# Optimization experiments

Hardware: AMD Instinct MI355X
Metric: run time of the kernel (lower is better)

The kernel has to match this reference:

```python
import jax, jax.numpy as jnp
import numpy as np

B, L, T, IN, H, OUT = 1024, 64, 128, 13, 64, 13
NEG = -1e30


def gru_step(x, h, Wih, Whh, bih, bhh):
    # PyTorch GRU cell: gates ordered (r, z, n)
    gi = x @ Wih.T + bih          # [B, 3H]
    gh = h @ Whh.T + bhh          # [B, 3H]
    ir, iz, inn = jnp.split(gi, 3, axis=-1)
    hr, hz, hn = jnp.split(gh, 3, axis=-1)
    r = jax.nn.sigmoid(ir + hr)
    z = jax.nn.sigmoid(iz + hz)
    n = jnp.tanh(inn + r * hn)
    return (1.0 - z) * n + z * h


def setup_inputs() -> dict:
    key = jax.random.key(0)
    ks = jax.random.split(key, 10)
    s = float(1.0 / np.sqrt(H))
    x = jax.random.normal(ks[0], (B, L, IN), jnp.float32)
    lengths = jax.random.randint(ks[1], (B,), 1, L + 1).at[0].set(L)
    Wih = jax.random.uniform(ks[2], (3 * H, IN), jnp.float32, -s, s)
    Whh = jax.random.uniform(ks[3], (3 * H, H), jnp.float32, -s, s)
    bih = jax.random.uniform(ks[4], (3 * H,), jnp.float32, -s, s)
    bhh = jax.random.uniform(ks[5], (3 * H,), jnp.float32, -s, s)
    Wf = jax.random.uniform(ks[6], (OUT, H), jnp.float32, -s, s)
    bf = jax.random.uniform(ks[7], (OUT,), jnp.float32, -s, s)
    Wa = jax.random.uniform(ks[8], (H, H), jnp.float32, -s, s)
    ba = jax.random.uniform(ks[9], (H,), jnp.float32, -s, s)
    return dict(x=x, lengths=lengths, output_length=T, Wih=Wih, Whh=Whh,
                bih=bih, bhh=bhh, Wf=Wf, bf=bf, Wa=Wa, ba=ba)


def reference(x, lengths, output_length, Wih, Whh, bih, bhh, Wf, bf, Wa, ba):
    b, l = x.shape[0], x.shape[1]
    xT = jnp.swapaxes(x, 0, 1)                        # [L, B, IN]
    h0 = jnp.zeros((b, H), x.dtype)

    # Encoder: masked GRU emulating pack_padded/pad_packed semantics:
    # hidden frozen past each sequence's length; outputs zero past length.
    def enc(h, inp):
        t, xt = inp
        hn = gru_step(xt, h, Wih, Whh, bih, bhh)
        valid = (t < lengths)[:, None]
        h = jnp.where(valid, hn, h)
        return h, jnp.where(valid, hn, 0.0)

    h, outs = jax.lax.scan(enc, h0, (jnp.arange(l), xT))
    # output[:, -1, :] of the padded output (zeros for seqs shorter than max)
    nin = outs[-1] @ Wf.T + bf                        # [B, OUT]

    Tn = output_length
    buf0 = jnp.zeros((Tn, b, H), x.dtype)             # growing past-prediction buffer

    def dec(carry, t):
        h, buf, nin = carry
        hn = gru_step(nin, h, Wih, Whh, bih, bhh)     # output_lstm == hidden (1 layer, 1 step)
        # attention recomputed over all past predictions (softmax over time axis)
        logits = jnp.einsum('tbh,gh->tbg', buf, Wa) + ba      # [T, B, H]
        logits = jnp.where((jnp.arange(Tn) < t)[:, None, None], logits, NEG)
        w = jax.nn.softmax(logits, axis=0)
        o = hn + jnp.sum(w * buf, axis=0)             # at t=0 buffer is all zeros -> +0
        y = o @ Wf.T + bf
        return (hn, buf.at[t].set(o), y), y

    _, ys = jax.lax.scan(dec, (h, buf0, nin), jnp.arange(Tn))
    return jnp.swapaxes(ys, 0, 1)                     # [B, T, OUT]
```

## Files before the change

### kernel.cpp

```cpp
#include <hip/hip_runtime.h>
#include <stdint.h>
#include <math.h>

#define BATCH 1024
#define SEQL  64
#define TDEC  128
#define NIN   13
#define NH    64
#define NOUT  13

typedef _Float16 h2 __attribute__((ext_vector_type(2)));
typedef __fp16   g2 __attribute__((ext_vector_type(2)));

union FU  { uint32_t u; float f; };
union HU  { uint16_t u; _Float16 h; };
union H2U { uint32_t u; h2 h; g2 g; };

__device__ __forceinline__ float bf2f(uint16_t v) { FU t; t.u = ((uint32_t)v) << 16; return t.f; }
__device__ __forceinline__ float hf2f(uint16_t v) { HU t; t.u = v; return (float)t.h; }

__device__ __forceinline__ float ldf(const void* p, long i, int mode) {
    if (mode == 1) return bf2f(((const uint16_t*)p)[i]);
    if (mode == 2) return hf2f(((const uint16_t*)p)[i]);
    return ((const float*)p)[i];
}

__device__ __forceinline__ bool pass_stats(const void* p, int n, int lane, int mode,
                                           float band_lo, float band_hi, float max_ok) {
    int m = (n + 1) / 2;
    int cnt = (m < 64) ? m : 64;
    bool ok_max = true, in_band = false;
    if (lane < cnt) {
        long pos = 2L * (((long)lane * m) / cnt);
        float v = (mode == 1) ? bf2f(((const uint16_t*)p)[pos])
                              : hf2f(((const uint16_t*)p)[pos]);
        float a = fabsf(v);
        ok_max  = (a <= max_ok);
        in_band = (a >= band_lo && a <= band_hi);
    }
    bool allmax = __all(ok_max);
    int nb = (int)__popcll(__ballot(in_band));
    int need = cnt / 4; if (need < 1) need = 1;
    return allmax && (nb >= need);
}
__device__ __forceinline__ int detect(const void* p, int n, int lane,
                                      float band_lo, float band_hi, float max_ok) {
    if (pass_stats(p, n, lane, 1, band_lo, band_hi, max_ok)) return 1;
    if (pass_stats(p, n, lane, 2, band_lo, band_hi, max_ok)) return 2;
    return 0;
}
__device__ __forceinline__ bool detect_len64(const int* p, int lane) {
    int v = p[2 * lane + 1];
    return __all(v == 0);
}

__device__ __forceinline__ float dot2(h2 a, h2 b, float c) {
#if __has_builtin(__builtin_amdgcn_fdot2)
    return __builtin_amdgcn_fdot2(a, b, c, false);
#else
    return c + (float)a[0] * (float)b[0] + (float)a[1] * (float)b[1];
#endif
}
__device__ __forceinline__ uint32_t pku(float a, float b) {
    H2U t; t.g = __builtin_amdgcn_cvt_pkrtz(a, b); return t.u;
}
__device__ __forceinline__ h2 uh(uint32_t u) { H2U t; t.u = u; return t.h; }
__device__ __forceinline__ float rcp_(float x) { return __builtin_amdgcn_rcpf(x); }
__device__ __forceinline__ float exp2_(float x) {
#if __has_builtin(__builtin_amdgcn_exp2f)
    return __builtin_amdgcn_exp2f(x);
#else
    return __expf(x * 0.69314718056f);
#endif
}
__device__ __forceinline__ float sigm2(float xs)  { return rcp_(1.0f + exp2_(-xs)); }
__device__ __forceinline__ float tanh2(float xs)  { return 1.0f - 2.0f * rcp_(exp2_(xs) + 1.0f); }

__device__ __forceinline__ float swap1(float v) {
    FU a; a.f = v;
    FU b; b.u = (uint32_t)__builtin_amdgcn_mov_dpp((int)a.u, 0xB1, 0xF, 0xF, true);
    return b.f;
}

#define BCAST32(vreg, dst)                                                 \
    {                                                                      \
        uint32_t _pr = pku((vreg), swap1(vreg));                           \
        _Pragma("unroll")                                                  \
        for (int _k = 0; _k < 32; ++_k)                                    \
            (dst)[_k] = __builtin_amdgcn_readlane(_pr, 2 * _k);            \
    }

__global__ __launch_bounds__(64, 1)
void gru_attn_kernel(const void* __restrict__ x, const int* __restrict__ lengths,
                     const void* __restrict__ Wih, const void* __restrict__ Whh,
                     const void* __restrict__ bih, const void* __restrict__ bhh,
                     const void* __restrict__ Wf, const void* __restrict__ bfv,
                     const void* __restrict__ Wa, const void* __restrict__ ba,
                     float* __restrict__ out)
{
    const int b = blockIdx.x;
    const int j = threadIdx.x;

    const int dX   = detect(x,   BATCH * SEQL * NIN, j, 0.25f, 4.0f, 16.0f);
    const int dWih = detect(Wih, 3 * NH * NIN, j, 0.04f, 0.13f, 0.14f);
    const int dWhh = detect(Whh, 3 * NH * NH,  j, 0.04f, 0.13f, 0.14f);
    const int dBih = detect(bih, 3 * NH,       j, 0.04f, 0.13f, 0.14f);
    const int dBhh = detect(bhh, 3 * NH,       j, 0.04f, 0.13f, 0.14f);
    const int dWf  = detect(Wf,  NOUT * NH,    j, 0.04f, 0.13f, 0.14f);
    const int dBf  = detect(bfv, NOUT,         j, 0.04f, 0.13f, 0.14f);
    const int dWa  = detect(Wa,  NH * NH,      j, 0.04f, 0.13f, 0.14f);
    const int dBa  = detect(ba,  NH,           j, 0.04f, 0.13f, 0.14f);
    const bool len64 = detect_len64(lengths, j);

    const float L2E  = 1.44269504089f;
    const float L2E2 = 2.88539008177f;

    h2 wihr[7], wihz[7], wihn[7];
    h2 whhr[32], whhz[32], whhn[32];
    h2 wap[32], wfp[32];

#pragma unroll
    for (int k = 0; k < 7; ++k) {
        float a0 = ldf(Wih, (0 * NH + j) * NIN + 2 * k, dWih);
        float a1 = (2 * k + 1 < NIN) ? ldf(Wih, (0 * NH + j) * NIN + 2 * k + 1, dWih) : 0.0f;
        wihr[k] = uh(pku(a0 * L2E, a1 * L2E));
        float b0 = ldf(Wih, (1 * NH + j) * NIN + 2 * k, dWih);
        float b1 = (2 * k + 1 < NIN) ? ldf(Wih, (1 * NH + j) * NIN + 2 * k + 1, dWih) : 0.0f;
        wihz[k] = uh(pku(b0 * L2E, b1 * L2E));
        float c0 = ldf(Wih, (2 * NH + j) * NIN + 2 * k, dWih);
        float c1 = (2 * k + 1 < NIN) ? ldf(Wih, (2 * NH + j) * NIN + 2 * k + 1, dWih) : 0.0f;
        wihn[k] = uh(pku(c0 * L2E2, c1 * L2E2));
    }
    const int jf = (j < NOUT) ? j : 0;
#pragma unroll
    for (int k = 0; k < 32; ++k) {
        whhr[k] = uh(pku(ldf(Whh, (0 * NH + j) * NH + 2 * k, dWhh) * L2E,
                         ldf(Whh, (0 * NH + j) * NH + 2 * k + 1, dWhh) * L2E));
        whhz[k] = uh(pku(ldf(Whh, (1 * NH + j) * NH + 2 * k, dWhh) * L2E,
                         ldf(Whh, (1 * NH + j) * NH + 2 * k + 1, dWhh) * L2E));
        whhn[k] = uh(pku(ldf(Whh, (2 * NH + j) * NH + 2 * k, dWhh) * L2E2,
                         ldf(Whh, (2 * NH + j) * NH + 2 * k + 1, dWhh) * L2E2));
        wap[k]  = uh(pku(ldf(Wa, j * NH + 2 * k, dWa) * L2E,
                         ldf(Wa, j * NH + 2 * k + 1, dWa) * L2E));
        wfp[k]  = uh(pku(ldf(Wf, jf * NH + 2 * k, dWf),
                         ldf(Wf, jf * NH + 2 * k + 1, dWf)));
    }

    const float bcr = (ldf(bih, j, dBih)      + ldf(bhh, j, dBhh))      * L2E;
    const float bcz = (ldf(bih, NH + j, dBih) + ldf(bhh, NH + j, dBhh)) * L2E;
    const float bni = ldf(bih, 2 * NH + j, dBih) * L2E2;
    const float bnh = ldf(bhh, 2 * NH + j, dBhh) * L2E2;
    const float baj = ldf(ba, j, dBa) * L2E;
    const float bfj = ldf(bfv, jf, dBf);
    const int len = len64 ? lengths[2 * b] : lengths[b];

    uint32_t xp[7];
    {
        const long base = ((long)b * SEQL + j) * NIN;
        float v[14];
#pragma unroll
        for (int k = 0; k < NIN; ++k) v[k] = ldf(x, base + k, dX);
        v[13] = 0.0f;
#pragma unroll
        for (int p = 0; p < 7; ++p) xp[p] = pku(v[2 * p], v[2 * p + 1]);
    }

    float h = 0.0f;
    float out_last = 0.0f;

    uint32_t hpk[32];
#pragma unroll
    for (int k = 0; k < 32; ++k) hpk[k] = 0u;

    float gir, giz, gin;
    {
        uint32_t xw[7];
#pragma unroll
        for (int p = 0; p < 7; ++p) xw[p] = __builtin_amdgcn_readlane(xp[p], 0);
        float r0 = 0.0f, z0 = 0.0f, n0 = 0.0f;
#pragma unroll
        for (int p = 0; p < 7; ++p) {
            h2 xv = uh(xw[p]);
            r0 = dot2(wihr[p], xv, r0);
            z0 = dot2(wihz[p], xv, z0);
            n0 = dot2(wihn[p], xv, n0);
        }
        gir = r0; giz = z0; gin = n0;
    }

#pragma unroll 1
    for (int t = 0; t < SEQL; ++t) {
        float arA = bcr, azA = bcz, hnA = bnh;
        float arB = 0.0f, azB = 0.0f, hnB = 0.0f;
        float arC = 0.0f, azC = 0.0f, hnC = 0.0f;
        float arD = 0.0f, azD = 0.0f, hnD = 0.0f;
#pragma unroll
        for (int k = 0; k < 32; k += 4) {
            h2 h0 = uh(hpk[k]), h1 = uh(hpk[k + 1]), h2v = uh(hpk[k + 2]), h3 = uh(hpk[k + 3]);
            arA = dot2(whhr[k],     h0, arA); azA = dot2(whhz[k],     h0, azA); hnA = dot2(whhn[k],     h0, hnA);
            arB = dot2(whhr[k + 1], h1, arB); azB = dot2(whhz[k + 1], h1, azB); hnB = dot2(whhn[k + 1], h1, hnB);
            arC = dot2(whhr[k + 2], h2v, arC); azC = dot2(whhz[k + 2], h2v, azC); hnC = dot2(whhn[k + 2], h2v, hnC);
            arD = dot2(whhr[k + 3], h3, arD); azD = dot2(whhz[k + 3], h3, azD); hnD = dot2(whhn[k + 3], h3, hnD);
        }

        float girN = 0.0f, gizN = 0.0f, ginN = 0.0f;
        {
            uint32_t xwN[7];
#pragma unroll
            for (int p = 0; p < 7; ++p)
                xwN[p] = __builtin_amdgcn_readlane(xp[p], (t + 1) & 63);
#pragma unroll
            for (int p = 0; p < 7; ++p) {
                h2 xv = uh(xwN[p]);
                girN = dot2(wihr[p], xv, girN);
                gizN = dot2(wihz[p], xv, gizN);
                ginN = dot2(wihn[p], xv, ginN);
            }
        }

        float ar = ((arA + arB) + (arC + arD)) + gir;
        float az = ((azA + azB) + (azC + azD)) + giz;
        float hna = (hnA + hnB) + (hnC + hnD);
        float an = bni + gin;
        float r = sigm2(ar);
        float z = sigm2(az);
        float n = tanh2(an + r * hna);
        float hnew = n + z * (h - n);
        bool upd = (t < len);
        h = upd ? hnew : h;
        if (t == SEQL - 1) out_last = upd ? hnew : 0.0f;
        BCAST32(h, hpk);
        gir = girN; giz = gizN; gin = ginN;
    }

    uint32_t ypk0[7];
    {
        uint32_t opk[32];
        BCAST32(out_last, opk);
        float nA = bfj, nB = 0.0f, nC = 0.0f, nD = 0.0f;
#pragma unroll
        for (int k = 0; k < 32; k += 4) {
            nA = dot2(wfp[k],     uh(opk[k]),     nA);
            nB = dot2(wfp[k + 1], uh(opk[k + 1]), nB);
            nC = dot2(wfp[k + 2], uh(opk[k + 2]), nC);
            nD = dot2(wfp[k + 3], uh(opk[k + 3]), nD);
        }
        float nv = (nA + nB) + (nC + nD);
        float nz = (j < NOUT) ? nv : 0.0f;
        uint32_t pr = pku(nz, swap1(nz));
#pragma unroll
        for (int k = 0; k < 7; ++k) ypk0[k] = __builtin_amdgcn_readlane(pr, 2 * k);
    }

    float m = -1e30f, Zs = 0.0f, num = 0.0f;
    float o_prev;

    {
        float arA = bcr, azA = bcz, hnA = bnh, anA = bni;
        float arB = 0.0f, azB = 0.0f, hnB = 0.0f;
        float arC = 0.0f, azC = 0.0f, hnC = 0.0f;
        float arD = 0.0f, azD = 0.0f, hnD = 0.0f;
#pragma unroll
        for (int k = 0; k < 32; k += 4) {
            h2 h0 = uh(hpk[k]), h1 = uh(hpk[k + 1]), h2v = uh(hpk[k + 2]), h3 = uh(hpk[k + 3]);
            arA = dot2(whhr[k],     h0, arA); azA = dot2(whhz[k],     h0, azA); hnA = dot2(whhn[k],     h0, hnA);
            arB = dot2(whhr[k + 1], h1, arB); azB = dot2(whhz[k + 1], h1, azB); hnB = dot2(whhn[k + 1], h1, hnB);
            arC = dot2(whhr[k + 2], h2v, arC); azC = dot2(whhz[k + 2], h2v, azC); hnC = dot2(whhn[k + 2], h2v, hnC);
            arD = dot2(whhr[k + 3], h3, arD); azD = dot2(whhz[k + 3], h3, azD); hnD = dot2(whhn[k + 3], h3, hnD);
        }
#pragma unroll
        for (int p = 0; p < 7; ++p) {
            h2 xv = uh(ypk0[p]);
            arB = dot2(wihr[p], xv, arB);
            azB = dot2(wihz[p], xv, azB);
            anA = dot2(wihn[p], xv, anA);
        }
        float ar = (arA + arB) + (arC + arD);
        float az = (azA + azB) + (azC + azD);
        float hna = (hnA + hnB) + (hnC + hnD);
        float r = sigm2(ar);
        float z = sigm2(az);
        float n = tanh2(anA + r * hna);
        float hnew = n + z * (h - n);
        h = hnew;
        BCAST32(hnew, hpk);
        o_prev = hnew;
    }

#pragma unroll 1
    for (int t = 1; t < TDEC; ++t) {
        uint32_t opk[32];
        BCAST32(o_prev, opk);

        float arA = bcr, azA = bcz, hnA = bnh, anA = bni;
        float arB = 0.0f, azB = 0.0f, hnB = 0.0f;
        float arC = 0.0f, azC = 0.0f, hnC = 0.0f;
        float arD = 0.0f, azD = 0.0f, hnD = 0.0f;
#pragma unroll
        for (int k = 0; k < 32; k += 4) {
            h2 h0 = uh(hpk[k]), h1 = uh(hpk[k + 1]), h2v = uh(hpk[k + 2]), h3 = uh(hpk[k + 3]);
            arA = dot2(whhr[k],     h0, arA); azA = dot2(whhz[k],     h0, azA); hnA = dot2(whhn[k],     h0, hnA);
            arB = dot2(whhr[k + 1], h1, arB); azB = dot2(whhz[k + 1], h1, azB); hnB = dot2(whhn[k + 1], h1, hnB);
            arC = dot2(whhr[k + 2], h2v, arC); azC = dot2(whhz[k + 2], h2v, azC); hnC = dot2(whhn[k + 2], h2v, hnC);
            arD = dot2(whhr[k + 3], h3, arD); azD = dot2(whhz[k + 3], h3, azD); hnD = dot2(whhn[k + 3], h3, hnD);
        }

        float yA = bfj, yB = 0.0f, yC = 0.0f, yD = 0.0f;
#pragma unroll
        for (int k = 0; k < 32; k += 4) {
            yA = dot2(wfp[k],     uh(opk[k]),     yA);
            yB = dot2(wfp[k + 1], uh(opk[k + 1]), yB);
            yC = dot2(wfp[k + 2], uh(opk[k + 2]), yC);
            yD = dot2(wfp[k + 3], uh(opk[k + 3]), yD);
        }
        float yv = (yA + yB) + (yC + yD);
        if (j < NOUT) out[((size_t)b * TDEC + (t - 1)) * NOUT + j] = yv;

        uint32_t ypk[7];
        {
            float yz = (j < NOUT) ? yv : 0.0f;
            uint32_t pr = pku(yz, swap1(yz));
#pragma unroll
            for (int k = 0; k < 7; ++k) ypk[k] = __builtin_amdgcn_readlane(pr, 2 * k);
        }
#pragma unroll
        for (int p = 0; p < 7; ++p) {
            h2 xv = uh(ypk[p]);
            arB = dot2(wihr[p], xv, arB);
            azB = dot2(wihz[p], xv, azB);
            anA = dot2(wihn[p], xv, anA);
        }

        float sA = baj, sB = 0.0f, sC = 0.0f, sD = 0.0f;
#pragma unroll
        for (int k = 0; k < 32; k += 4) {
            sA = dot2(wap[k],     uh(opk[k]),     sA);
            sB = dot2(wap[k + 1], uh(opk[k + 1]), sB);
            sC = dot2(wap[k + 2], uh(opk[k + 2]), sC);
            sD = dot2(wap[k + 3], uh(opk[k + 3]), sD);
        }
        float s_ = (sA + sB) + (sC + sD);
        float mn = fmaxf(m, s_);
        float al = exp2_(m - mn);
        float pp = exp2_(s_ - mn);
        Zs  = Zs * al + pp;
        num = num * al + pp * o_prev;
        m = mn;

        float ar = (arA + arB) + (arC + arD);
        float az = (azA + azB) + (azC + azD);
        float hna = (hnA + hnB) + (hnC + hnD);
        float r_ = sigm2(ar);
        float z_ = sigm2(az);
        float n_ = tanh2(anA + r_ * hna);
        float hnew = n_ + z_ * (h - n_);
        h = hnew;

        float attn = num * rcp_(Zs);
        float o_ = hnew + attn;
        BCAST32(hnew, hpk);
        o_prev = o_;
    }

    {
        uint32_t opk[32];
        BCAST32(o_prev, opk);
        float yA = bfj, yB = 0.0f, yC = 0.0f, yD = 0.0f;
#pragma unroll
        for (int k = 0; k < 32; k += 4) {
            yA = dot2(wfp[k],     uh(opk[k]),     yA);
            yB = dot2(wfp[k + 1], uh(opk[k + 1]), yB);
            yC = dot2(wfp[k + 2], uh(opk[k + 2]), yC);
            yD = dot2(wfp[k + 3], uh(opk[k + 3]), yD);
        }
        float yv = (yA + yB) + (yC + yD);
        if (j < NOUT) out[((size_t)b * TDEC + (TDEC - 1)) * NOUT + j] = yv;
    }
}

extern "C" void kernel_launch(void* const* d_in, const int* in_sizes, int n_in,
                              void* d_out, int out_size, void* d_ws, size_t ws_size,
                              hipStream_t stream) {
    (void)in_sizes; (void)n_in; (void)out_size; (void)d_ws; (void)ws_size;
    const void* x      = d_in[0];
    const int* lengths = (const int*)d_in[1];
    const void* Wih = d_in[3];
    const void* Whh = d_in[4];
    const void* bih = d_in[5];
    const void* bhh = d_in[6];
    const void* Wf  = d_in[7];
    const void* bf  = d_in[8];
    const void* Wa  = d_in[9];
    const void* ba  = d_in[10];
    float* out = (float*)d_out;

    gru_attn_kernel<<<dim3(BATCH), dim3(64), 0, stream>>>(
        x, lengths, Wih, Whh, bih, bhh, Wf, bf, Wa, ba, out);
}
```

Baseline: 231.4 us.

## Broadcast decoder output via LDS and interleave attention/output dots with recurrence

Replaces the readlane broadcast of each decoder step's output with packed fp16 writes to a small shared-memory buffer read back as vector loads. The half-precision dot products for the attention score and output projection are interleaved with the recurrent dot products. The encoder loop is simplified to compute the input projection inline with unroll 2 instead of software-pipelining it. The intent is to cut the 32 serial readlanes per decoder step and improve instruction-level parallelism, but no barrier is placed between the LDS write and the next read. That relies on single-wave execution and risks a race.

```diff
diff --git a/kernel.cpp b/kernel.cpp
--- a/kernel.cpp
+++ b/kernel.cpp
@@ -90,6 +90,23 @@
             (dst)[_k] = __builtin_amdgcn_readlane(_pr, 2 * _k);            \
     }
 
+#define BWRITE(DSTB, V)                                                    \
+    {                                                                      \
+        float _w  = swap1(V);                                              \
+        float _lo = odd ? _w  : (V);                                       \
+        float _hi = odd ? (V) : _w;                                        \
+        (DSTB)[jhalf] = pku(_lo, _hi);                                     \
+    }
+#define BREAD(SRC, DST)                                                    \
+    {                                                                      \
+        _Pragma("unroll")                                                  \
+        for (int _k = 0; _k < 32; _k += 4) {                               \
+            uint4 _q = *(const uint4*)((SRC) + _k);                        \
+            (DST)[_k]     = _q.x; (DST)[_k + 1] = _q.y;                    \
+            (DST)[_k + 2] = _q.z; (DST)[_k + 3] = _q.w;                    \
+        }                                                                  \
+    }
+
 __global__ __launch_bounds__(64, 1)
 void gru_attn_kernel(const void* __restrict__ x, const int* __restrict__ lengths,
                      const void* __restrict__ Wih, const void* __restrict__ Whh,
@@ -100,6 +117,10 @@
 {
     const int b = blockIdx.x;
     const int j = threadIdx.x;
+    const bool odd = j & 1;
+    const int jhalf = j >> 1;
+
+    __shared__ __align__(16) uint32_t ob[32];
 
     const int dX   = detect(x,   BATCH * SEQL * NIN, j, 0.25f, 4.0f, 16.0f);
     const int dWih = detect(Wih, 3 * NH * NIN, j, 0.04f, 0.13f, 0.14f);
@@ -169,28 +190,15 @@
     float out_last = 0.0f;
 
     uint32_t hpk[32];
-#pragma unroll
-    for (int k = 0; k < 32; ++k) hpk[k] = 0u;
-
-    float gir, giz, gin;
-    {
+    BCAST32(h, hpk);
+
+#pragma unroll 2
+    for (int t = 0; t < SEQL; ++t) {
         uint32_t xw[7];
 #pragma unroll
-        for (int p = 0; p < 7; ++p) xw[p] = __builtin_amdgcn_readlane(xp[p], 0);
-        float r0 = 0.0f, z0 = 0.0f, n0 = 0.0f;
-#pragma unroll
-        for (int p = 0; p < 7; ++p) {
-            h2 xv = uh(xw[p]);
-            r0 = dot2(wihr[p], xv, r0);
-            z0 = dot2(wihz[p], xv, z0);
-            n0 = dot2(wihn[p], xv, n0);
-        }
-        gir = r0; giz = z0; gin = n0;
-    }
-
-#pragma unroll 1
-    for (int t = 0; t < SEQL; ++t) {
-        float arA = bcr, azA = bcz, hnA = bnh;
+        for (int p = 0; p < 7; ++p) xw[p] = __builtin_amdgcn_readlane(xp[p], t);
+
+        float arA = bcr, azA = bcz, hnA = bnh, anA = bni;
         float arB = 0.0f, azB = 0.0f, hnB = 0.0f;
         float arC = 0.0f, azC = 0.0f, hnC = 0.0f;
         float arD = 0.0f, azD = 0.0f, hnD = 0.0f;
@@ -202,38 +210,27 @@
             arC = dot2(whhr[k + 2], h2v, arC); azC = dot2(whhz[k + 2], h2v, azC); hnC = dot2(whhn[k + 2], h2v, hnC);
             arD = dot2(whhr[k + 3], h3, arD); azD = dot2(whhz[k + 3], h3, azD); hnD = dot2(whhn[k + 3], h3, hnD);
         }
-
-        float girN = 0.0f, gizN = 0.0f, ginN = 0.0f;
-        {
-            uint32_t xwN[7];
-#pragma unroll
-            for (int p = 0; p < 7; ++p)
-                xwN[p] = __builtin_amdgcn_readlane(xp[p], (t + 1) & 63);
-#pragma unroll
-            for (int p = 0; p < 7; ++p) {
-                h2 xv = uh(xwN[p]);
-                girN = dot2(wihr[p], xv, girN);
-                gizN = dot2(wihz[p], xv, gizN);
-                ginN = dot2(wihn[p], xv, ginN);
-            }
-        }
-
-        float ar = ((arA + arB) + (arC + arD)) + gir;
-        float az = ((azA + azB) + (azC + azD)) + giz;
+#pragma unroll
+        for (int p = 0; p < 7; ++p) {
+            h2 xv = uh(xw[p]);
+            arB = dot2(wihr[p], xv, arB);
+            azB = dot2(wihz[p], xv, azB);
+            anA = dot2(wihn[p], xv, anA);
+        }
+        float ar = (arA + arB) + (arC + arD);
+        float az = (azA + azB) + (azC + azD);
         float hna = (hnA + hnB) + (hnC + hnD);
-        float an = bni + gin;
         float r = sigm2(ar);
         float z = sigm2(az);
-        float n = tanh2(an + r * hna);
+        float n = tanh2(anA + r * hna);
         float hnew = n + z * (h - n);
         bool upd = (t < len);
         h = upd ? hnew : h;
         if (t == SEQL - 1) out_last = upd ? hnew : 0.0f;
         BCAST32(h, hpk);
-        gir = girN; giz = gizN; gin = ginN;
-    }
-
-    uint32_t ypk0[7];
+    }
+
+    uint32_t ypk[7];
     {
         uint32_t opk[32];
         BCAST32(out_last, opk);
@@ -249,7 +246,7 @@
         float nz = (j < NOUT) ? nv : 0.0f;
         uint32_t pr = pku(nz, swap1(nz));
 #pragma unroll
-        for (int k = 0; k < 7; ++k) ypk0[k] = __builtin_amdgcn_readlane(pr, 2 * k);
+        for (int k = 0; k < 7; ++k) ypk[k] = __builtin_amdgcn_readlane(pr, 2 * k);
     }
 
     float m = -1e30f, Zs = 0.0f, num = 0.0f;
@@ -270,7 +267,7 @@
         }
 #pragma unroll
         for (int p = 0; p < 7; ++p) {
-            h2 xv = uh(ypk0[p]);
+            h2 xv = uh(ypk[p]);
             arB = dot2(wihr[p], xv, arB);
             azB = dot2(wihz[p], xv, azB);
             anA = dot2(wihn[p], xv, anA);
@@ -285,19 +282,21 @@
         h = hnew;
         BCAST32(hnew, hpk);
         o_prev = hnew;
+        BWRITE(ob, o_prev);
     }
 
 #pragma unroll 1
-    for (int t = 1; t < TDEC; ++t) {
+    for (int t = 0; t < TDEC - 1; ++t) {
         uint32_t opk[32];
-        BCAST32(o_prev, opk);
+        BREAD(ob, opk);
 
         float arA = bcr, azA = bcz, hnA = bnh, anA = bni;
         float arB = 0.0f, azB = 0.0f, hnB = 0.0f;
         float arC = 0.0f, azC = 0.0f, hnC = 0.0f;
         float arD = 0.0f, azD = 0.0f, hnD = 0.0f;
-#pragma unroll
-        for (int k = 0; k < 32; k += 4) {
+
+#pragma unroll
+        for (int k = 0; k < 16; k += 4) {
             h2 h0 = uh(hpk[k]), h1 = uh(hpk[k + 1]), h2v = uh(hpk[k + 2]), h3 = uh(hpk[k + 3]);
             arA = dot2(whhr[k],     h0, arA); azA = dot2(whhz[k],     h0, azA); hnA = dot2(whhn[k],     h0, hnA);
             arB = dot2(whhr[k + 1], h1, arB); azB = dot2(whhz[k + 1], h1, azB); hnB = dot2(whhn[k + 1], h1, hnB);
@@ -305,24 +304,47 @@
             arD = dot2(whhr[k + 3], h3, arD); azD = dot2(whhz[k + 3], h3, azD); hnD = dot2(whhn[k + 3], h3, hnD);
         }
 
+        float sA = baj, sB = 0.0f, sC = 0.0f, sD = 0.0f;
         float yA = bfj, yB = 0.0f, yC = 0.0f, yD = 0.0f;
-#pragma unroll
-        for (int k = 0; k < 32; k += 4) {
+
+#pragma unroll
+        for (int k = 16; k < 32; k += 4) {
+            const int k2 = k - 16;
+            h2 h0 = uh(hpk[k]), h1 = uh(hpk[k + 1]), h2v = uh(hpk[k + 2]), h3 = uh(hpk[k + 3]);
+            h2 o0 = uh(opk[k2]), o1 = uh(opk[k2 + 1]), o2 = uh(opk[k2 + 2]), o3 = uh(opk[k2 + 3]);
+            arA = dot2(whhr[k],     h0, arA); azA = dot2(whhz[k],     h0, azA); hnA = dot2(whhn[k],     h0, hnA);
+            sA = dot2(wap[k2],     o0, sA);  yA = dot2(wfp[k2],     o0, yA);
+            arB = dot2(whhr[k + 1], h1, arB); azB = dot2(whhz[k + 1], h1, azB); hnB = dot2(whhn[k + 1], h1, hnB);
+            sB = dot2(wap[k2 + 1], o1, sB);  yB = dot2(wfp[k2 + 1], o1, yB);
+            arC = dot2(whhr[k + 2], h2v, arC); azC = dot2(whhz[k + 2], h2v, azC); hnC = dot2(whhn[k + 2], h2v, hnC);
+            sC = dot2(wap[k2 + 2], o2, sC);  yC = dot2(wfp[k2 + 2], o2, yC);
+            arD = dot2(whhr[k + 3], h3, arD); azD = dot2(whhz[k + 3], h3, azD); hnD = dot2(whhn[k + 3], h3, hnD);
+            sD = dot2(wap[k2 + 3], o3, sD);  yD = dot2(wfp[k2 + 3], o3, yD);
+        }
+
+#pragma unroll
+        for (int k = 16; k < 32; k += 4) {
             yA = dot2(wfp[k],     uh(opk[k]),     yA);
             yB = dot2(wfp[k + 1], uh(opk[k + 1]), yB);
             yC = dot2(wfp[k + 2], uh(opk[k + 2]), yC);
             yD = dot2(wfp[k + 3], uh(opk[k + 3]), yD);
         }
         float yv = (yA + yB) + (yC + yD);
-        if (j < NOUT) out[((size_t)b * TDEC + (t - 1)) * NOUT + j] = yv;
-
-        uint32_t ypk[7];
         {
             float yz = (j < NOUT) ? yv : 0.0f;
             uint32_t pr = pku(yz, swap1(yz));
 #pragma unroll
             for (int k = 0; k < 7; ++k) ypk[k] = __builtin_amdgcn_readlane(pr, 2 * k);
         }
+
+#pragma unroll
+        for (int k = 16; k < 32; k += 4) {
+            sA = dot2(wap[k],     uh(opk[k]),     sA);
+            sB = dot2(wap[k + 1], uh(opk[k + 1]), sB);
+            sC = dot2(wap[k + 2], uh(opk[k + 2]), sC);
+            sD = dot2(wap[k + 3], uh(opk[k + 3]), sD);
+        }
+
 #pragma unroll
         for (int p = 0; p < 7; ++p) {
             h2 xv = uh(ypk[p]);
@@ -331,14 +353,6 @@
             anA = dot2(wihn[p], xv, anA);
         }
 
-        float sA = baj, sB = 0.0f, sC = 0.0f, sD = 0.0f;
-#pragma unroll
-        for (int k = 0; k < 32; k += 4) {
-            sA = dot2(wap[k],     uh(opk[k]),     sA);
-            sB = dot2(wap[k + 1], uh(opk[k + 1]), sB);
-            sC = dot2(wap[k + 2], uh(opk[k + 2]), sC);
-            sD = dot2(wap[k + 3], uh(opk[k + 3]), sD);
-        }
         float s_ = (sA + sB) + (sC + sD);
         float mn = fmaxf(m, s_);
         float al = exp2_(m - mn);
@@ -346,6 +360,7 @@
         Zs  = Zs * al + pp;
         num = num * al + pp * o_prev;
         m = mn;
+        float attn = num * rcp_(Zs);
 
         float ar = (arA + arB) + (arC + arD);
         float az = (azA + azB) + (azC + azD);
@@ -356,15 +371,17 @@
         float hnew = n_ + z_ * (h - n_);
         h = hnew;
 
-        float attn = num * rcp_(Zs);
         float o_ = hnew + attn;
         BCAST32(hnew, hpk);
+        BWRITE(ob, o_);
         o_prev = o_;
+
+        if (j < NOUT) out[((size_t)b * TDEC + t) * NOUT + j] = yv;
     }
 
     {
         uint32_t opk[32];
-        BCAST32(o_prev, opk);
+        BREAD(ob, opk);
         float yA = bfj, yB = 0.0f, yC = 0.0f, yD = 0.0f;
 #pragma unroll
         for (int k = 0; k < 32; k += 4) {
```

New measurement: 218.5 us. -5.6%, faster.

## Split hidden-dim reduction across two wavefronts with LDS partial-sum exchange

Applied to the files above, without the earlier changes.

Each block now runs two wavefronts, and each one handles half of the 64-wide hidden input dimension for the recurrent, attention and output matvecs. Partial sums are swapped through a double-buffered shared-memory array with a __syncthreads each step. This halves the per-thread dot-product and readlane broadcast work on the serial recurrence critical path. In exchange it adds a block barrier and an LDS round trip per timestep, and it drops the encoder's one-step-ahead input-projection prefetch.

```diff
diff --git a/kernel.cpp b/kernel.cpp
--- a/kernel.cpp
+++ b/kernel.cpp
@@ -82,15 +82,15 @@
     return b.f;
 }
 
-#define BCAST32(vreg, dst)                                                 \
+#define PACKHALF(vreg, dst)                                                \
     {                                                                      \
         uint32_t _pr = pku((vreg), swap1(vreg));                           \
         _Pragma("unroll")                                                  \
-        for (int _k = 0; _k < 32; ++_k)                                    \
-            (dst)[_k] = __builtin_amdgcn_readlane(_pr, 2 * _k);            \
-    }
-
-__global__ __launch_bounds__(64, 1)
+        for (int _k = 0; _k < 16; ++_k)                                    \
+            (dst)[_k] = __builtin_amdgcn_readlane(_pr, kb + 2 * _k);       \
+    }
+
+__global__ __launch_bounds__(128, 1)
 void gru_attn_kernel(const void* __restrict__ x, const int* __restrict__ lengths,
                      const void* __restrict__ Wih, const void* __restrict__ Whh,
                      const void* __restrict__ bih, const void* __restrict__ bhh,
@@ -98,8 +98,12 @@
                      const void* __restrict__ Wa, const void* __restrict__ ba,
                      float* __restrict__ out)
 {
-    const int b = blockIdx.x;
-    const int j = threadIdx.x;
+    const int b  = blockIdx.x;
+    const int j  = threadIdx.x & 63;
+    const int w  = threadIdx.x >> 6;
+    const int kb = w << 5;
+
+    __shared__ __align__(16) float xch[2][2][64][8];
 
     const int dX   = detect(x,   BATCH * SEQL * NIN, j, 0.25f, 4.0f, 16.0f);
     const int dWih = detect(Wih, 3 * NH * NIN, j, 0.04f, 0.13f, 0.14f);
@@ -116,8 +120,8 @@
     const float L2E2 = 2.88539008177f;
 
     h2 wihr[7], wihz[7], wihn[7];
-    h2 whhr[32], whhz[32], whhn[32];
-    h2 wap[32], wfp[32];
+    h2 whhr[16], whhz[16], whhn[16];
+    h2 wap[16], wfp[16];
 
 #pragma unroll
     for (int k = 0; k < 7; ++k) {
@@ -133,17 +137,18 @@
     }
     const int jf = (j < NOUT) ? j : 0;
 #pragma unroll
-    for (int k = 0; k < 32; ++k) {
-        whhr[k] = uh(pku(ldf(Whh, (0 * NH + j) * NH + 2 * k, dWhh) * L2E,
-                         ldf(Whh, (0 * NH + j) * NH + 2 * k + 1, dWhh) * L2E));
-        whhz[k] = uh(pku(ldf(Whh, (1 * NH + j) * NH + 2 * k, dWhh) * L2E,
-                         ldf(Whh, (1 * NH + j) * NH + 2 * k + 1, dWhh) * L2E));
-        whhn[k] = uh(pku(ldf(Whh, (2 * NH + j) * NH + 2 * k, dWhh) * L2E2,
-                         ldf(Whh, (2 * NH + j) * NH + 2 * k + 1, dWhh) * L2E2));
-        wap[k]  = uh(pku(ldf(Wa, j * NH + 2 * k, dWa) * L2E,
-                         ldf(Wa, j * NH + 2 * k + 1, dWa) * L2E));
-        wfp[k]  = uh(pku(ldf(Wf, jf * NH + 2 * k, dWf),
-                         ldf(Wf, jf * NH + 2 * k + 1, dWf)));
+    for (int k = 0; k < 16; ++k) {
+        const int c = kb + 2 * k;
+        whhr[k] = uh(pku(ldf(Whh, (0 * NH + j) * NH + c, dWhh) * L2E,
+                         ldf(Whh, (0 * NH + j) * NH + c + 1, dWhh) * L2E));
+        whhz[k] = uh(pku(ldf(Whh, (1 * NH + j) * NH + c, dWhh) * L2E,
+                         ldf(Whh, (1 * NH + j) * NH + c + 1, dWhh) * L2E));
+        whhn[k] = uh(pku(ldf(Whh, (2 * NH + j) * NH + c, dWhh) * L2E2,
+                         ldf(Whh, (2 * NH + j) * NH + c + 1, dWhh) * L2E2));
+        wap[k]  = uh(pku(ldf(Wa, j * NH + c, dWa) * L2E,
+                         ldf(Wa, j * NH + c + 1, dWa) * L2E));
+        wfp[k]  = uh(pku(ldf(Wf, jf * NH + c, dWf),
+                         ldf(Wf, jf * NH + c + 1, dWf)));
     }
 
     const float bcr = (ldf(bih, j, dBih)      + ldf(bhh, j, dBhh))      * L2E;
@@ -167,214 +172,224 @@
 
     float h = 0.0f;
     float out_last = 0.0f;
-
-    uint32_t hpk[32];
-#pragma unroll
-    for (int k = 0; k < 32; ++k) hpk[k] = 0u;
-
-    float gir, giz, gin;
-    {
-        uint32_t xw[7];
-#pragma unroll
-        for (int p = 0; p < 7; ++p) xw[p] = __builtin_amdgcn_readlane(xp[p], 0);
-        float r0 = 0.0f, z0 = 0.0f, n0 = 0.0f;
-#pragma unroll
-        for (int p = 0; p < 7; ++p) {
-            h2 xv = uh(xw[p]);
-            r0 = dot2(wihr[p], xv, r0);
-            z0 = dot2(wihz[p], xv, z0);
-            n0 = dot2(wihn[p], xv, n0);
-        }
-        gir = r0; giz = z0; gin = n0;
-    }
+    int par = 0;
+
+    uint32_t hpk[16];
+#pragma unroll
+    for (int k = 0; k < 16; ++k) hpk[k] = 0u;
 
 #pragma unroll 1
     for (int t = 0; t < SEQL; ++t) {
-        float arA = bcr, azA = bcz, hnA = bnh;
-        float arB = 0.0f, azB = 0.0f, hnB = 0.0f;
-        float arC = 0.0f, azC = 0.0f, hnC = 0.0f;
-        float arD = 0.0f, azD = 0.0f, hnD = 0.0f;
-#pragma unroll
-        for (int k = 0; k < 32; k += 4) {
+        uint32_t xw[7];
+#pragma unroll
+        for (int p = 0; p < 7; ++p) xw[p] = __builtin_amdgcn_readlane(xp[p], t);
+
+        float arA = 0.f, azA = 0.f, hnA = 0.f;
+        float arB = 0.f, azB = 0.f, hnB = 0.f;
+        float arC = 0.f, azC = 0.f, hnC = 0.f;
+        float arD = 0.f, azD = 0.f, hnD = 0.f;
+#pragma unroll
+        for (int k = 0; k < 16; k += 4) {
             h2 h0 = uh(hpk[k]), h1 = uh(hpk[k + 1]), h2v = uh(hpk[k + 2]), h3 = uh(hpk[k + 3]);
             arA = dot2(whhr[k],     h0, arA); azA = dot2(whhz[k],     h0, azA); hnA = dot2(whhn[k],     h0, hnA);
             arB = dot2(whhr[k + 1], h1, arB); azB = dot2(whhz[k + 1], h1, azB); hnB = dot2(whhn[k + 1], h1, hnB);
             arC = dot2(whhr[k + 2], h2v, arC); azC = dot2(whhz[k + 2], h2v, azC); hnC = dot2(whhn[k + 2], h2v, hnC);
             arD = dot2(whhr[k + 3], h3, arD); azD = dot2(whhz[k + 3], h3, azD); hnD = dot2(whhn[k + 3], h3, hnD);
         }
-
-        float girN = 0.0f, gizN = 0.0f, ginN = 0.0f;
-        {
-            uint32_t xwN[7];
-#pragma unroll
-            for (int p = 0; p < 7; ++p)
-                xwN[p] = __builtin_amdgcn_readlane(xp[p], (t + 1) & 63);
-#pragma unroll
-            for (int p = 0; p < 7; ++p) {
-                h2 xv = uh(xwN[p]);
-                girN = dot2(wihr[p], xv, girN);
-                gizN = dot2(wihz[p], xv, gizN);
-                ginN = dot2(wihn[p], xv, ginN);
-            }
-        }
-
-        float ar = ((arA + arB) + (arC + arD)) + gir;
-        float az = ((azA + azB) + (azC + azD)) + giz;
-        float hna = (hnA + hnB) + (hnC + hnD);
-        float an = bni + gin;
+        float gr = bcr, gz = bcz, gn = bni;
+#pragma unroll
+        for (int p = 0; p < 7; ++p) {
+            h2 xv = uh(xw[p]);
+            gr = dot2(wihr[p], xv, gr);
+            gz = dot2(wihz[p], xv, gz);
+            gn = dot2(wihn[p], xv, gn);
+        }
+
+        float arP = (arA + arB) + (arC + arD);
+        float azP = (azA + azB) + (azC + azD);
+        float hnP = (hnA + hnB) + (hnC + hnD);
+        *(float4*)&xch[par][w][j][0] = make_float4(arP, azP, hnP, 0.f);
+        __syncthreads();
+        float4 q = *(const float4*)&xch[par][w ^ 1][j][0];
+        par ^= 1;
+
+        float ar  = (arP + q.x) + gr;
+        float az  = (azP + q.y) + gz;
+        float hna = (hnP + q.z) + bnh;
         float r = sigm2(ar);
         float z = sigm2(az);
-        float n = tanh2(an + r * hna);
+        float n = tanh2(gn + r * hna);
         float hnew = n + z * (h - n);
         bool upd = (t < len);
         h = upd ? hnew : h;
         if (t == SEQL - 1) out_last = upd ? hnew : 0.0f;
-        BCAST32(h, hpk);
-        gir = girN; giz = gizN; gin = ginN;
-    }
-
-    uint32_t ypk0[7];
+        PACKHALF(h, hpk);
+    }
+
+    uint32_t ypk[7];
     {
-        uint32_t opk[32];
-        BCAST32(out_last, opk);
-        float nA = bfj, nB = 0.0f, nC = 0.0f, nD = 0.0f;
-#pragma unroll
-        for (int k = 0; k < 32; k += 4) {
-            nA = dot2(wfp[k],     uh(opk[k]),     nA);
-            nB = dot2(wfp[k + 1], uh(opk[k + 1]), nB);
-            nC = dot2(wfp[k + 2], uh(opk[k + 2]), nC);
-            nD = dot2(wfp[k + 3], uh(opk[k + 3]), nD);
-        }
-        float nv = (nA + nB) + (nC + nD);
+        uint32_t olk[16];
+        PACKHALF(out_last, olk);
+        float nA = 0.f, nB = 0.f, nC = 0.f, nD = 0.f;
+#pragma unroll
+        for (int k = 0; k < 16; k += 4) {
+            nA = dot2(wfp[k],     uh(olk[k]),     nA);
+            nB = dot2(wfp[k + 1], uh(olk[k + 1]), nB);
+            nC = dot2(wfp[k + 2], uh(olk[k + 2]), nC);
+            nD = dot2(wfp[k + 3], uh(olk[k + 3]), nD);
+        }
+        float nP = (nA + nB) + (nC + nD);
+        xch[par][w][j][0] = nP;
+        __syncthreads();
+        float qn = xch[par][w ^ 1][j][0];
+        par ^= 1;
+        float nv = (nP + qn) + bfj;
         float nz = (j < NOUT) ? nv : 0.0f;
         uint32_t pr = pku(nz, swap1(nz));
 #pragma unroll
-        for (int k = 0; k < 7; ++k) ypk0[k] = __builtin_amdgcn_readlane(pr, 2 * k);
+        for (int k = 0; k < 7; ++k) ypk[k] = __builtin_amdgcn_readlane(pr, 2 * k);
     }
 
     float m = -1e30f, Zs = 0.0f, num = 0.0f;
     float o_prev;
+    uint32_t opk[16];
 
     {
-        float arA = bcr, azA = bcz, hnA = bnh, anA = bni;
-        float arB = 0.0f, azB = 0.0f, hnB = 0.0f;
-        float arC = 0.0f, azC = 0.0f, hnC = 0.0f;
-        float arD = 0.0f, azD = 0.0f, hnD = 0.0f;
-#pragma unroll
-        for (int k = 0; k < 32; k += 4) {
+        float arA = 0.f, azA = 0.f, hnA = 0.f;
+        float arB = 0.f, azB = 0.f, hnB = 0.f;
+        float arC = 0.f, azC = 0.f, hnC = 0.f;
+        float arD = 0.f, azD = 0.f, hnD = 0.f;
+#pragma unroll
+        for (int k = 0; k < 16; k += 4) {
             h2 h0 = uh(hpk[k]), h1 = uh(hpk[k + 1]), h2v = uh(hpk[k + 2]), h3 = uh(hpk[k + 3]);
             arA = dot2(whhr[k],     h0, arA); azA = dot2(whhz[k],     h0, azA); hnA = dot2(whhn[k],     h0, hnA);
             arB = dot2(whhr[k + 1], h1, arB); azB = dot2(whhz[k + 1], h1, azB); hnB = dot2(whhn[k + 1], h1, hnB);
             arC = dot2(whhr[k + 2], h2v, arC); azC = dot2(whhz[k + 2], h2v, azC); hnC = dot2(whhn[k + 2], h2v, hnC);
             arD = dot2(whhr[k + 3], h3, arD); azD = dot2(whhz[k + 3], h3, azD); hnD = dot2(whhn[k + 3], h3, hnD);
         }
+        float gr = bcr, gz = bcz, gn = bni;
 #pragma unroll
         for (int p = 0; p < 7; ++p) {
-            h2 xv = uh(ypk0[p]);
-            arB = dot2(wihr[p], xv, arB);
-            azB = dot2(wihz[p], xv, azB);
-            anA = dot2(wihn[p], xv, anA);
-        }
-        float ar = (arA + arB) + (arC + arD);
-        float az = (azA + azB) + (azC + azD);
-        float hna = (hnA + hnB) + (hnC + hnD);
+            h2 xv = uh(ypk[p]);
+            gr = dot2(wihr[p], xv, gr);
+            gz = dot2(wihz[p], xv, gz);
+            gn = dot2(wihn[p], xv, gn);
+        }
+        float arP = (arA + arB) + (arC + arD);
+        float azP = (azA + azB) + (azC + azD);
+        float hnP = (hnA + hnB) + (hnC + hnD);
+        *(float4*)&xch[par][w][j][0] = make_float4(arP, azP, hnP, 0.f);
+        __syncthreads();
+        float4 q = *(const float4*)&xch[par][w ^ 1][j][0];
+        par ^= 1;
+        float ar  = (arP + q.x) + gr;
+        float az  = (azP + q.y) + gz;
+        float hna = (hnP + q.z) + bnh;
         float r = sigm2(ar);
         float z = sigm2(az);
-        float n = tanh2(anA + r * hna);
+        float n = tanh2(gn + r * hna);
         float hnew = n + z * (h - n);
         h = hnew;
-        BCAST32(hnew, hpk);
         o_prev = hnew;
+        PACKHALF(hnew, hpk);
+        PACKHALF(o_prev, opk);
     }
 
 #pragma unroll 1
     for (int t = 1; t < TDEC; ++t) {
-        uint32_t opk[32];
-        BCAST32(o_prev, opk);
-
-        float arA = bcr, azA = bcz, hnA = bnh, anA = bni;
-        float arB = 0.0f, azB = 0.0f, hnB = 0.0f;
-        float arC = 0.0f, azC = 0.0f, hnC = 0.0f;
-        float arD = 0.0f, azD = 0.0f, hnD = 0.0f;
-#pragma unroll
-        for (int k = 0; k < 32; k += 4) {
+        float arA = 0.f, azA = 0.f, hnA = 0.f;
+        float arB = 0.f, azB = 0.f, hnB = 0.f;
+        float arC = 0.f, azC = 0.f, hnC = 0.f;
+        float arD = 0.f, azD = 0.f, hnD = 0.f;
+#pragma unroll
+        for (int k = 0; k < 16; k += 4) {
             h2 h0 = uh(hpk[k]), h1 = uh(hpk[k + 1]), h2v = uh(hpk[k + 2]), h3 = uh(hpk[k + 3]);
             arA = dot2(whhr[k],     h0, arA); azA = dot2(whhz[k],     h0, azA); hnA = dot2(whhn[k],     h0, hnA);
             arB = dot2(whhr[k + 1], h1, arB); azB = dot2(whhz[k + 1], h1, azB); hnB = dot2(whhn[k + 1], h1, hnB);
             arC = dot2(whhr[k + 2], h2v, arC); azC = dot2(whhz[k + 2], h2v, azC); hnC = dot2(whhn[k + 2], h2v, hnC);
             arD = dot2(whhr[k + 3], h3, arD); azD = dot2(whhz[k + 3], h3, azD); hnD = dot2(whhn[k + 3], h3, hnD);
         }
-
-        float yA = bfj, yB = 0.0f, yC = 0.0f, yD = 0.0f;
-#pragma unroll
-        for (int k = 0; k < 32; k += 4) {
-            yA = dot2(wfp[k],     uh(opk[k]),     yA);
-            yB = dot2(wfp[k + 1], uh(opk[k + 1]), yB);
-            yC = dot2(wfp[k + 2], uh(opk[k + 2]), yC);
-            yD = dot2(wfp[k + 3], uh(opk[k + 3]), yD);
-        }
-        float yv = (yA + yB) + (yC + yD);
-        if (j < NOUT) out[((size_t)b * TDEC + (t - 1)) * NOUT + j] = yv;
-
-        uint32_t ypk[7];
+        float sA = 0.f, sB = 0.f, sC = 0.f, sD = 0.f;
+        float yA = 0.f, yB = 0.f, yC = 0.f, yD = 0.f;
+#pragma unroll
+        for (int k = 0; k < 16; k += 4) {
+            h2 o0 = uh(opk[k]), o1 = uh(opk[k + 1]), o2 = uh(opk[k + 2]), o3 = uh(opk[k + 3]);
+            sA = dot2(wap[k],     o0, sA); yA = dot2(wfp[k],     o0, yA);
+            sB = dot2(wap[k + 1], o1, sB); yB = dot2(wfp[k + 1], o1, yB);
+            sC = dot2(wap[k + 2], o2, sC); yC = dot2(wfp[k + 2], o2, yC);
+            sD = dot2(wap[k + 3], o3, sD); yD = dot2(wfp[k + 3], o3, yD);
+        }
+        float arP = (arA + arB) + (arC + arD);
+        float azP = (azA + azB) + (azC + azD);
+        float hnP = (hnA + hnB) + (hnC + hnD);
+        float sP  = (sA + sB) + (sC + sD);
+        float yP  = (yA + yB) + (yC + yD);
+        {
+            float* wrb = &xch[par][w][j][0];
+            *(float4*)wrb = make_float4(arP, azP, hnP, sP);
+            wrb[4] = yP;
+        }
+        __syncthreads();
+        const float* rb = &xch[par][w ^ 1][j][0];
+        float4 q = *(const float4*)rb;
+        float qy = rb[4];
+        par ^= 1;
+
+        float yv = (yP + qy) + bfj;
+        if (w == 0 && j < NOUT) out[((size_t)b * TDEC + (t - 1)) * NOUT + j] = yv;
         {
             float yz = (j < NOUT) ? yv : 0.0f;
             uint32_t pr = pku(yz, swap1(yz));
 #pragma unroll
             for (int k = 0; k < 7; ++k) ypk[k] = __builtin_amdgcn_readlane(pr, 2 * k);
         }
-#pragma unroll
-        for (int p = 0; p < 7; ++p) {
-            h2 xv = uh(ypk[p]);
-            arB = dot2(wihr[p], xv, arB);
-            azB = dot2(wihz[p], xv, azB);
-            anA = dot2(wihn[p], xv, anA);
-        }
-
-        float sA = baj, sB = 0.0f, sC = 0.0f, sD = 0.0f;
-#pragma unroll
-        for (int k = 0; k < 32; k += 4) {
-            sA = dot2(wap[k],     uh(opk[k]),     sA);
-            sB = dot2(wap[k + 1], uh(opk[k + 1]), sB);
-            sC = dot2(wap[k + 2], uh(opk[k + 2]), sC);
-            sD = dot2(wap[k + 3], uh(opk[k + 3]), sD);
-        }
-        float s_ = (sA + sB) + (sC + sD);
+
+        float s_ = (sP + q.w) + baj;
         float mn = fmaxf(m, s_);
         float al = exp2_(m - mn);
         float pp = exp2_(s_ - mn);
         Zs  = Zs * al + pp;
         num = num * al + pp * o_prev;
         m = mn;
-
-        float ar = (arA + arB) + (arC + arD);
-        float az = (azA + azB) + (azC + azD);
-        float hna = (hnA + hnB) + (hnC + hnD);
+        float attn = num * rcp_(Zs);
+
+        float gr = bcr, gz = bcz, gn = bni;
+#pragma unroll
+        for (int p = 0; p < 7; ++p) {
+            h2 xv = uh(ypk[p]);
+            gr = dot2(wihr[p], xv, gr);
+            gz = dot2(wihz[p], xv, gz);
+            gn = dot2(wihn[p], xv, gn);
+        }
+        float ar  = (arP + q.x) + gr;
+        float az  = (azP + q.y) + gz;
+        float hna = (hnP + q.z) + bnh;
         float r_ = sigm2(ar);
         float z_ = sigm2(az);
-        float n_ = tanh2(anA + r_ * hna);
+        float n_ = tanh2(gn + r_ * hna);
         float hnew = n_ + z_ * (h - n_);
         h = hnew;
-
-        float attn = num * rcp_(Zs);
         float o_ = hnew + attn;
-        BCAST32(hnew, hpk);
         o_prev = o_;
+        PACKHALF(hnew, hpk);
+        PACKHALF(o_, opk);
     }
 
     {
-        uint32_t opk[32];
-        BCAST32(o_prev, opk);
-        float yA = bfj, yB = 0.0f, yC = 0.0f, yD = 0.0f;
-#pragma unroll
-        for (int k = 0; k < 32; k += 4) {
+        float yA = 0.f, yB = 0.f, yC = 0.f, yD = 0.f;
+#pragma unroll
+        for (int k = 0; k < 16; k += 4) {
             yA = dot2(wfp[k],     uh(opk[k]),     yA);
             yB = dot2(wfp[k + 1], uh(opk[k + 1]), yB);
             yC = dot2(wfp[k + 2], uh(opk[k + 2]), yC);
             yD = dot2(wfp[k + 3], uh(opk[k + 3]), yD);
         }
-        float yv = (yA + yB) + (yC + yD);
-        if (j < NOUT) out[((size_t)b * TDEC + (TDEC - 1)) * NOUT + j] = yv;
+        float yP = (yA + yB) + (yC + yD);
+        xch[par][w][j][0] = yP;
+        __syncthreads();
+        float qy = xch[par][w ^ 1][j][0];
+        float yv = (yP + qy) + bfj;
+        if (w == 0 && j < NOUT) out[((size_t)b * TDEC + (TDEC - 1)) * NOUT + j] = yv;
     }
 }
 
@@ -394,6 +409,6 @@
     const void* ba  = d_in[10];
     float* out = (float*)d_out;
 
-    gru_attn_kernel<<<dim3(BATCH), dim3(64), 0, stream>>>(
+    gru_attn_kernel<<<dim3(BATCH), dim3(128), 0, stream>>>(
         x, lengths, Wih, Whh, bih, bhh, Wf, bf, Wa, ba, out);
 }
```

Result: slower. 317.0 us (+37.0%).
